# Kernel optimization log

Hardware: AMD Instinct MI355X
Metric: run time of the kernel (lower is better)

## Reference

```python
import jax, jax.numpy as jnp
import numpy as np

N_NODES = 100000


def _gcn_conv(x, row, col, W, b, n):
    # PyG GCNConv: h = W x; out_i = sum_{j->i} norm_ij * h_j + b, with self-loops
    # and symmetric normalization norm_ij = deg_i^-1/2 * deg_j^-1/2.
    h = x @ W  # [N, out]
    loop = jnp.arange(n, dtype=row.dtype)
    r = jnp.concatenate([row, loop])
    c = jnp.concatenate([col, loop])
    deg = jax.ops.segment_sum(jnp.ones_like(c, dtype=h.dtype), c, num_segments=n)
    dinv = jnp.where(deg > 0, jax.lax.rsqrt(deg), 0.0)
    norm = dinv[r] * dinv[c]  # [E+N]
    msg = h[r] * norm[:, None]  # gather + per-edge scale
    out = jax.ops.segment_sum(msg, c, num_segments=n)  # scatter-add to dst
    return out + b


def setup_inputs() -> dict:
    key = jax.random.key(0)
    ks = jax.random.split(key, 8)
    N, E = N_NODES, 1600000
    d_in, comm_dim, hid, out = 120, 8, 128, 64
    x = jax.random.normal(ks[0], (N, d_in), dtype=jnp.float32)
    edge_index = jax.random.randint(ks[1], (2, E), 0, N, dtype=jnp.int64)
    comm_ids = jax.random.randint(ks[2], (N,), 0, 64, dtype=jnp.int64)
    comm_emb = jax.random.normal(ks[3], (64, comm_dim), dtype=jnp.float32)
    s1 = 1.0 / np.sqrt(d_in + comm_dim)
    s2 = 1.0 / np.sqrt(hid)
    W1 = jax.random.normal(ks[4], (d_in + comm_dim, hid), dtype=jnp.float32) * s1
    b1 = jnp.zeros((hid,), dtype=jnp.float32)
    W2 = jax.random.normal(ks[5], (hid, out), dtype=jnp.float32) * s2
    b2 = jnp.zeros((out,), dtype=jnp.float32)
    return {"x": x, "edge_index": edge_index, "comm_ids": comm_ids,
            "comm_emb": comm_emb, "W1": W1, "b1": b1, "W2": W2, "b2": b2}


def reference(x, edge_index, comm_ids, comm_emb, W1, b1, W2, b2):
    n = x.shape[0]
    row, col = edge_index[0], edge_index[1]
    c = comm_emb[comm_ids]                      # [N, comm_dim] embedding lookup
    h = jnp.concatenate([x, c], axis=-1)        # [N, in+comm_dim]
    h = jax.nn.relu(_gcn_conv(h, row, col, W1, b1, n))
    # dropout p=0.5 is inactive in eval mode (training=False)
    out = _gcn_conv(h, row, col, W2, b2, n)     # [N, out_channels]
    return out
```

## Files before the change

kernel.cpp:

```cpp
#include <hip/hip_runtime.h>

typedef __attribute__((ext_vector_type(8))) short bf16x8;
typedef __attribute__((ext_vector_type(4))) float f32x4;

#define CAPB 5632
#define NBMAX 512

static __device__ __forceinline__ unsigned short f2bf(float f) {
    unsigned u = __float_as_uint(f);
    unsigned r = (u + 0x7fff + ((u >> 16) & 1)) >> 16;
    return (unsigned short)r;
}
static __device__ __forceinline__ float bfu_lo(unsigned v) { return __uint_as_float(v << 16); }
static __device__ __forceinline__ float bfu_hi(unsigned v) { return __uint_as_float(v & 0xffff0000u); }

static __device__ __forceinline__ bf16x8 cvt8(float4 u0, float4 u1) {
    bf16x8 r;
    r[0] = (short)f2bf(u0.x); r[1] = (short)f2bf(u0.y);
    r[2] = (short)f2bf(u0.z); r[3] = (short)f2bf(u0.w);
    r[4] = (short)f2bf(u1.x); r[5] = (short)f2bf(u1.y);
    r[6] = (short)f2bf(u1.z); r[7] = (short)f2bf(u1.w);
    return r;
}

__global__ void k_zero_int(int* __restrict__ p, int n) {
    int i = blockIdx.x * blockDim.x + threadIdx.x;
    if (i < n) p[i] = 0;
}

__global__ __launch_bounds__(256) void k_passA(const int* __restrict__ row,
                                               const int* __restrict__ col,
                                               int* __restrict__ gcnt,
                                               unsigned long long* __restrict__ packed,
                                               int E, int NB) {
    __shared__ int lcnt[NBMAX];
    __shared__ int lbase[NBMAX];
    __shared__ int lcur[NBMAX];
    __shared__ int gbaseS[NBMAX];
    __shared__ unsigned long long stage[4096];
    __shared__ int s[256];

    int tid = threadIdx.x;
    int t0 = blockIdx.x * 4096;
    int total = min(4096, E - t0);

    for (int b = tid; b < NBMAX; b += 256) { lcnt[b] = 0; lcur[b] = 0; }
    __syncthreads();

    int er[16], ec[16];
#pragma unroll
    for (int j = 0; j < 16; ++j) {
        int e = t0 + j * 256 + tid;
        if (e < E) {
            er[j] = row[e];
            ec[j] = col[e];
            atomicAdd(&lcnt[ec[j] >> 8], 1);
        }
    }
    __syncthreads();

    int c0 = lcnt[2 * tid], c1 = lcnt[2 * tid + 1];
    int p = c0 + c1;
    s[tid] = p;
    __syncthreads();
    for (int off = 1; off < 256; off <<= 1) {
        int t = (tid >= off) ? s[tid - off] : 0;
        __syncthreads();
        s[tid] += t;
        __syncthreads();
    }
    int ebase = s[tid] - p;
    lbase[2 * tid] = ebase;
    lbase[2 * tid + 1] = ebase + c0;
    __syncthreads();

    for (int b = tid; b < NB; b += 256) {
        int lc = lcnt[b];
        if (lc > 0) gbaseS[b] = atomicAdd(&gcnt[b], lc);
    }
    __syncthreads();

#pragma unroll
    for (int j = 0; j < 16; ++j) {
        int e = t0 + j * 256 + tid;
        if (e < E) {
            int b = ec[j] >> 8;
            int pos = lbase[b] + atomicAdd(&lcur[b], 1);
            stage[pos] = ((unsigned long long)(unsigned)er[j] << 32) | (unsigned)ec[j];
        }
    }
    __syncthreads();

    for (int j = tid; j < total; j += 256) {
        unsigned long long v = stage[j];
        int b = ((int)(unsigned)v) >> 8;
        packed[(size_t)b * CAPB + gbaseS[b] + (j - lbase[b])] = v;
    }
}

__global__ void k_bscan(const int* __restrict__ gcnt, int* __restrict__ gbase,
                        int* __restrict__ indptr, int n, int E, int NB) {
    __shared__ int s[512];
    int tid = threadIdx.x;
    int v = (tid < NB) ? gcnt[tid] : 0;
    s[tid] = v;
    __syncthreads();
    for (int off = 1; off < 512; off <<= 1) {
        int t = (tid >= off) ? s[tid - off] : 0;
        __syncthreads();
        s[tid] += t;
        __syncthreads();
    }
    if (tid < NB) gbase[tid] = s[tid] - v;
    if (tid == 0) indptr[n] = E;
}

__global__ __launch_bounds__(256) void k_passB(const unsigned long long* __restrict__ packed,
                                               const int* __restrict__ gcnt,
                                               const int* __restrict__ gbase,
                                               int* __restrict__ indptr,
                                               float* __restrict__ dinv,
                                               int* __restrict__ srcidx, int n) {
    __shared__ int ncnt[256];
    __shared__ int nbase[256];
    __shared__ int srow[CAPB];

    int b = blockIdx.x;
    int tid = threadIdx.x;
    int nodeBase = b << 8;
    int cntE = min(gcnt[b], CAPB);
    int base = gbase[b];
    size_t pb = (size_t)b * CAPB;

    ncnt[tid] = 0;
    __syncthreads();

    for (int j = tid; j < cntE; j += 256) {
        int c = (int)(unsigned)packed[pb + j];
        atomicAdd(&ncnt[c & 255], 1);
    }
    __syncthreads();

    int v = ncnt[tid];
    nbase[tid] = v;
    __syncthreads();
    for (int off = 1; off < 256; off <<= 1) {
        int t = (tid >= off) ? nbase[tid - off] : 0;
        __syncthreads();
        nbase[tid] += t;
        __syncthreads();
    }
    int excl = nbase[tid] - v;
    __syncthreads();
    nbase[tid] = excl;

    int node = nodeBase + tid;
    if (node < n) {
        indptr[node] = base + excl;
        dinv[node] = rsqrtf((float)(v + 1));
    }
    ncnt[tid] = 0;
    __syncthreads();

    for (int j = tid; j < cntE; j += 256) {
        unsigned long long e = packed[pb + j];
        int c = ((int)(unsigned)e) & 255;
        int r = (int)(e >> 32);
        int p = nbase[c] + atomicAdd(&ncnt[c], 1);
        srow[p] = r;
    }
    __syncthreads();

    for (int j = tid; j < cntE; j += 256) srcidx[base + j] = srow[j];
}

__global__ void k_wprep(const float* __restrict__ W, unsigned short* __restrict__ Wt,
                        int nout) {
    int idx = blockIdx.x * blockDim.x + threadIdx.x;
    if (idx >= nout * 128) return;
    int colc = idx >> 7, k = idx & 127;
    Wt[colc * 128 + k] = f2bf(W[k * nout + colc]);
}

__global__ __launch_bounds__(256) void k_gemm1(const float* __restrict__ x,
                                               const int* __restrict__ cid,
                                               const float* __restrict__ cemb,
                                               const unsigned short* __restrict__ Wt,
                                               const float* __restrict__ dinv,
                                               unsigned short* __restrict__ D, int n) {
    int tid = threadIdx.x;
    int wid = tid >> 6, lane = tid & 63;
    int rbase = blockIdx.x * 64 + wid * 16;
    int lr = lane & 15, kq = lane >> 4;

    int arow = rbase + lr;
    if (arow > n - 1) arow = n - 1;
    const float* xp = x + (size_t)arow * 120 + kq * 8;

    bf16x8 a0 = cvt8(*(const float4*)(xp),      *(const float4*)(xp + 4));
    bf16x8 a1 = cvt8(*(const float4*)(xp + 32), *(const float4*)(xp + 36));
    bf16x8 a2 = cvt8(*(const float4*)(xp + 64), *(const float4*)(xp + 68));
    bf16x8 a3;
    if (kq < 3) {
        a3 = cvt8(*(const float4*)(xp + 96), *(const float4*)(xp + 100));
    } else {
        const float* cp = cemb + (size_t)cid[arow] * 8;
        a3 = cvt8(*(const float4*)(cp), *(const float4*)(cp + 4));
    }

    f32x4 acc[8];
#pragma unroll
    for (int cf = 0; cf < 8; ++cf) acc[cf] = (f32x4){0.f, 0.f, 0.f, 0.f};

#pragma unroll
    for (int cf = 0; cf < 8; ++cf) {
        const unsigned short* bp = Wt + (size_t)(cf * 16 + lr) * 128 + kq * 8;
        bf16x8 b0 = *(const bf16x8*)(bp);
        bf16x8 b1 = *(const bf16x8*)(bp + 32);
        bf16x8 b2 = *(const bf16x8*)(bp + 64);
        bf16x8 b3 = *(const bf16x8*)(bp + 96);
        acc[cf] = __builtin_amdgcn_mfma_f32_16x16x32_bf16(a0, b0, acc[cf], 0, 0, 0);
        acc[cf] = __builtin_amdgcn_mfma_f32_16x16x32_bf16(a1, b1, acc[cf], 0, 0, 0);
        acc[cf] = __builtin_amdgcn_mfma_f32_16x16x32_bf16(a2, b2, acc[cf], 0, 0, 0);
        acc[cf] = __builtin_amdgcn_mfma_f32_16x16x32_bf16(a3, b3, acc[cf], 0, 0, 0);
    }

    float dv[4];
#pragma unroll
    for (int r = 0; r < 4; ++r) {
        int grow = rbase + kq * 4 + r;
        dv[r] = (grow < n) ? dinv[grow] : 0.f;
    }
#pragma unroll
    for (int cf = 0; cf < 8; ++cf) {
#pragma unroll
        for (int r = 0; r < 4; ++r) {
            int grow = rbase + kq * 4 + r;
            if (grow < n) D[(size_t)grow * 128 + cf * 16 + lr] = f2bf(acc[cf][r] * dv[r]);
        }
    }
}

template <int NOUT>
__global__ __launch_bounds__(256) void k_gemm_bf16(const unsigned short* __restrict__ A,
                                                   const unsigned short* __restrict__ Wt,
                                                   const float* __restrict__ dinv,
                                                   unsigned short* __restrict__ D, int n) {
    constexpr int NCF = NOUT / 16;
    int tid = threadIdx.x;
    int wid = tid >> 6, lane = tid & 63;
    int rbase = blockIdx.x * 64 + wid * 16;
    int lr = lane & 15, kq = lane >> 4;

    int arow = rbase + lr;
    if (arow > n - 1) arow = n - 1;
    const unsigned short* ap = A + (size_t)arow * 128 + kq * 8;
    bf16x8 a0 = *(const bf16x8*)(ap);
    bf16x8 a1 = *(const bf16x8*)(ap + 32);
    bf16x8 a2 = *(const bf16x8*)(ap + 64);
    bf16x8 a3 = *(const bf16x8*)(ap + 96);

    f32x4 acc[NCF];
#pragma unroll
    for (int cf = 0; cf < NCF; ++cf) acc[cf] = (f32x4){0.f, 0.f, 0.f, 0.f};

#pragma unroll
    for (int cf = 0; cf < NCF; ++cf) {
        const unsigned short* bp = Wt + (size_t)(cf * 16 + lr) * 128 + kq * 8;
        bf16x8 b0 = *(const bf16x8*)(bp);
        bf16x8 b1 = *(const bf16x8*)(bp + 32);
        bf16x8 b2 = *(const bf16x8*)(bp + 64);
        bf16x8 b3 = *(const bf16x8*)(bp + 96);
        acc[cf] = __builtin_amdgcn_mfma_f32_16x16x32_bf16(a0, b0, acc[cf], 0, 0, 0);
        acc[cf] = __builtin_amdgcn_mfma_f32_16x16x32_bf16(a1, b1, acc[cf], 0, 0, 0);
        acc[cf] = __builtin_amdgcn_mfma_f32_16x16x32_bf16(a2, b2, acc[cf], 0, 0, 0);
        acc[cf] = __builtin_amdgcn_mfma_f32_16x16x32_bf16(a3, b3, acc[cf], 0, 0, 0);
    }

    float dv[4];
#pragma unroll
    for (int r = 0; r < 4; ++r) {
        int grow = rbase + kq * 4 + r;
        dv[r] = (grow < n) ? dinv[grow] : 0.f;
    }
#pragma unroll
    for (int cf = 0; cf < NCF; ++cf) {
#pragma unroll
        for (int r = 0; r < 4; ++r) {
            int grow = rbase + kq * 4 + r;
            if (grow < n) D[(size_t)grow * NOUT + cf * 16 + lr] = f2bf(acc[cf][r] * dv[r]);
        }
    }
}


__global__ __launch_bounds__(64) void k_agg1(const unsigned* __restrict__ Hs,
                                             const int* __restrict__ indptr,
                                             const int* __restrict__ srcidx,
                                             const float* __restrict__ dinv,
                                             const float* __restrict__ bias,
                                             unsigned* __restrict__ Out, int n) {
    int i = blockIdx.x;
    int lane = threadIdx.x;
    unsigned sv = Hs[(size_t)i * 64 + lane];
    float ax = bfu_lo(sv), ay = bfu_hi(sv);
    int e0 = indptr[i], e1 = indptr[i + 1];
#pragma unroll 4
    for (int e = e0; e < e1; ++e) {
        unsigned v = Hs[(size_t)srcidx[e] * 64 + lane];
        ax += bfu_lo(v);
        ay += bfu_hi(v);
    }
    float di = dinv[i];
    float2 b = *(const float2*)&bias[lane * 2];
    float ox = fmaxf(di * ax + b.x, 0.f);
    float oy = fmaxf(di * ay + b.y, 0.f);
    Out[(size_t)i * 64 + lane] = (unsigned)f2bf(ox) | ((unsigned)f2bf(oy) << 16);
}

__global__ __launch_bounds__(64) void k_agg2(const unsigned* __restrict__ Hs,
                                             const int* __restrict__ indptr,
                                             const int* __restrict__ srcidx,
                                             const float* __restrict__ dinv,
                                             const float* __restrict__ bias,
                                             float2* __restrict__ Out, int n) {
    int i = blockIdx.x;
    int lane = threadIdx.x;
    int v = lane & 31, h = lane >> 5;
    float ax = 0.f, ay = 0.f;
    if (h == 0) {
        unsigned sv = Hs[(size_t)i * 32 + v];
        ax = bfu_lo(sv); ay = bfu_hi(sv);
    }
    int e0 = indptr[i], e1 = indptr[i + 1];
#pragma unroll 4
    for (int e = e0 + h; e < e1; e += 2) {
        unsigned w = Hs[(size_t)srcidx[e] * 32 + v];
        ax += bfu_lo(w);
        ay += bfu_hi(w);
    }
    ax += __shfl_xor(ax, 32);
    ay += __shfl_xor(ay, 32);
    if (h == 0) {
        float di = dinv[i];
        float2 b = *(const float2*)&bias[v * 2];
        Out[(size_t)i * 32 + v] = make_float2(di * ax + b.x, di * ay + b.y);
    }
}


extern "C" void kernel_launch(void* const* d_in, const int* in_sizes, int n_in,
                              void* d_out, int out_size, void* d_ws, size_t ws_size,
                              hipStream_t stream) {
    const float* x    = (const float*)d_in[0];
    const int*   eidx = (const int*)d_in[1];
    const int*   cid  = (const int*)d_in[2];
    const float* cemb = (const float*)d_in[3];
    const float* W1   = (const float*)d_in[4];
    const float* b1   = (const float*)d_in[5];
    const float* W2   = (const float*)d_in[6];
    const float* b2   = (const float*)d_in[7];
    float* out = (float*)d_out;

    int n = in_sizes[2];
    int E = in_sizes[1] / 2;
    const int* row = eidx;
    const int* col = eidx + E;
    int NB = (n + 255) / 256;

    char* ws = (char*)d_ws;
    auto alloc = [&](size_t bytes) {
        char* p = ws;
        ws += (bytes + 255) & ~(size_t)255;
        return p;
    };
    float*              dinv   = (float*)alloc((size_t)n * 4);
    int*                gcnt   = (int*)alloc((size_t)NB * 4);
    int*                gbase  = (int*)alloc((size_t)NB * 4);
    int*                indptr = (int*)alloc((size_t)(n + 1) * 4);
    int*                srcidx = (int*)alloc((size_t)E * 4);
    unsigned long long* packed = (unsigned long long*)alloc((size_t)NB * CAPB * 8);
    unsigned short*     Wt1    = (unsigned short*)alloc(128 * 128 * 2);
    unsigned short*     Wt2    = (unsigned short*)alloc(64 * 128 * 2);
    unsigned short*     D1     = (unsigned short*)alloc((size_t)n * 128 * 2);
    unsigned short*     H1     = (unsigned short*)alloc((size_t)n * 128 * 2);
    unsigned short*     D2     = (unsigned short*)alloc((size_t)n * 64 * 2);

    k_zero_int<<<(NB + 255) / 256, 256, 0, stream>>>(gcnt, NB);
    k_passA<<<(E + 4095) / 4096, 256, 0, stream>>>(row, col, gcnt, packed, E, NB);
    k_bscan<<<1, 512, 0, stream>>>(gcnt, gbase, indptr, n, E, NB);
    k_passB<<<NB, 256, 0, stream>>>(packed, gcnt, gbase, indptr, dinv, srcidx, n);

    k_wprep<<<(128 * 128 + 255) / 256, 256, 0, stream>>>(W1, Wt1, 128);
    k_wprep<<<(64 * 128 + 255) / 256, 256, 0, stream>>>(W2, Wt2, 64);

    int gb = (n + 63) / 64;
    k_gemm1<<<gb, 256, 0, stream>>>(x, cid, cemb, Wt1, dinv, D1, n);
    k_agg1<<<n, 64, 0, stream>>>((const unsigned*)D1, indptr, srcidx, dinv, b1,
                                 (unsigned*)H1, n);
    k_gemm_bf16<64><<<gb, 256, 0, stream>>>(H1, Wt2, dinv, D2, n);
    k_agg2<<<n, 64, 0, stream>>>((const unsigned*)D2, indptr, srcidx, dinv, b2,
                                 (float2*)out, n);
}
```

Before: 225.3 us.

## Quantize layer-1 features to int8 with per-row scales and pack edges in 32 bits

The first GEMM now writes its dinv-scaled output as int8 with a per-row absmax scale instead of bf16. This halves the bytes that the layer-1 aggregation gathers per neighbor. The aggregation dequantizes on the fly, writes H1 in a permuted column order, and the W2 weights are permuted to match. Edge packing during the CSR build shrinks from 64-bit to 32-bit words (row<<8 | low col bits), and the two weight-prep launches are merged into one. The cost is lower precision in the layer-1 messages, which may hurt accuracy, plus an extra scale load per edge.

```diff
diff --git a/kernel.cpp b/kernel.cpp
--- a/kernel.cpp
+++ b/kernel.cpp
@@ -13,6 +13,9 @@
 }
 static __device__ __forceinline__ float bfu_lo(unsigned v) { return __uint_as_float(v << 16); }
 static __device__ __forceinline__ float bfu_hi(unsigned v) { return __uint_as_float(v & 0xffff0000u); }
+static __device__ __forceinline__ unsigned packbf(float a, float b) {
+    return (unsigned)f2bf(a) | ((unsigned)f2bf(b) << 16);
+}
 
 static __device__ __forceinline__ bf16x8 cvt8(float4 u0, float4 u1) {
     bf16x8 r;
@@ -31,13 +34,14 @@
 __global__ __launch_bounds__(256) void k_passA(const int* __restrict__ row,
                                                const int* __restrict__ col,
                                                int* __restrict__ gcnt,
-                                               unsigned long long* __restrict__ packed,
+                                               unsigned* __restrict__ packed,
                                                int E, int NB) {
     __shared__ int lcnt[NBMAX];
     __shared__ int lbase[NBMAX];
     __shared__ int lcur[NBMAX];
     __shared__ int gbaseS[NBMAX];
-    __shared__ unsigned long long stage[4096];
+    __shared__ unsigned stage[4096];
+    __shared__ unsigned short stageb[4096];
     __shared__ int s[256];
 
     int tid = threadIdx.x;
@@ -86,15 +90,15 @@
         if (e < E) {
             int b = ec[j] >> 8;
             int pos = lbase[b] + atomicAdd(&lcur[b], 1);
-            stage[pos] = ((unsigned long long)(unsigned)er[j] << 32) | (unsigned)ec[j];
+            stage[pos] = ((unsigned)er[j] << 8) | ((unsigned)ec[j] & 255u);
+            stageb[pos] = (unsigned short)b;
         }
     }
     __syncthreads();
 
     for (int j = tid; j < total; j += 256) {
-        unsigned long long v = stage[j];
-        int b = ((int)(unsigned)v) >> 8;
-        packed[(size_t)b * CAPB + gbaseS[b] + (j - lbase[b])] = v;
+        int b = stageb[j];
+        packed[(size_t)b * CAPB + gbaseS[b] + (j - lbase[b])] = stage[j];
     }
 }
 
@@ -115,7 +119,7 @@
     if (tid == 0) indptr[n] = E;
 }
 
-__global__ __launch_bounds__(256) void k_passB(const unsigned long long* __restrict__ packed,
+__global__ __launch_bounds__(256) void k_passB(const unsigned* __restrict__ packed,
                                                const int* __restrict__ gcnt,
                                                const int* __restrict__ gbase,
                                                int* __restrict__ indptr,
@@ -136,8 +140,8 @@
     __syncthreads();
 
     for (int j = tid; j < cntE; j += 256) {
-        int c = (int)(unsigned)packed[pb + j];
-        atomicAdd(&ncnt[c & 255], 1);
+        unsigned e = packed[pb + j];
+        atomicAdd(&ncnt[e & 255u], 1);
     }
     __syncthreads();
 
@@ -163,9 +167,9 @@
     __syncthreads();
 
     for (int j = tid; j < cntE; j += 256) {
-        unsigned long long e = packed[pb + j];
-        int c = ((int)(unsigned)e) & 255;
-        int r = (int)(e >> 32);
+        unsigned e = packed[pb + j];
+        int c = (int)(e & 255u);
+        int r = (int)(e >> 8);
         int p = nbase[c] + atomicAdd(&ncnt[c], 1);
         srow[p] = r;
     }
@@ -174,12 +178,18 @@
     for (int j = tid; j < cntE; j += 256) srcidx[base + j] = srow[j];
 }
 
-__global__ void k_wprep(const float* __restrict__ W, unsigned short* __restrict__ Wt,
-                        int nout) {
+__global__ void k_wprep(const float* __restrict__ W1, const float* __restrict__ W2,
+                        unsigned short* __restrict__ Wt1, unsigned short* __restrict__ Wt2p) {
     int idx = blockIdx.x * blockDim.x + threadIdx.x;
-    if (idx >= nout * 128) return;
-    int colc = idx >> 7, k = idx & 127;
-    Wt[colc * 128 + k] = f2bf(W[k * nout + colc]);
+    if (idx < 128 * 128) {
+        int colc = idx >> 7, k = idx & 127;
+        Wt1[colc * 128 + k] = f2bf(W1[k * 128 + colc]);
+    } else if (idx < 128 * 128 + 64 * 128) {
+        int j = idx - 128 * 128;
+        int colc = j >> 7, p = j & 127;
+        int korig = (p & 7) * 16 + (p >> 3);
+        Wt2p[colc * 128 + p] = f2bf(W2[korig * 64 + colc]);
+    }
 }
 
 __global__ __launch_bounds__(256) void k_gemm1(const float* __restrict__ x,
@@ -187,7 +197,8 @@
                                                const float* __restrict__ cemb,
                                                const unsigned short* __restrict__ Wt,
                                                const float* __restrict__ dinv,
-                                               unsigned short* __restrict__ D, int n) {
+                                               unsigned char* __restrict__ D1q,
+                                               float* __restrict__ scales, int n) {
     int tid = threadIdx.x;
     int wid = tid >> 6, lane = tid & 63;
     int rbase = blockIdx.x * 64 + wid * 16;
@@ -225,18 +236,32 @@
         acc[cf] = __builtin_amdgcn_mfma_f32_16x16x32_bf16(a3, b3, acc[cf], 0, 0, 0);
     }
 
-    float dv[4];
 #pragma unroll
     for (int r = 0; r < 4; ++r) {
         int grow = rbase + kq * 4 + r;
-        dv[r] = (grow < n) ? dinv[grow] : 0.f;
-    }
-#pragma unroll
-    for (int cf = 0; cf < 8; ++cf) {
-#pragma unroll
-        for (int r = 0; r < 4; ++r) {
-            int grow = rbase + kq * 4 + r;
-            if (grow < n) D[(size_t)grow * 128 + cf * 16 + lr] = f2bf(acc[cf][r] * dv[r]);
+        float dv = (grow < n) ? dinv[grow] : 0.f;
+        float m = 0.f;
+#pragma unroll
+        for (int cf = 0; cf < 8; ++cf) m = fmaxf(m, fabsf(acc[cf][r] * dv));
+        m = fmaxf(m, __shfl_xor(m, 1));
+        m = fmaxf(m, __shfl_xor(m, 2));
+        m = fmaxf(m, __shfl_xor(m, 4));
+        m = fmaxf(m, __shfl_xor(m, 8));
+        float sinv = (m > 1e-20f) ? 127.f / m : 0.f;
+        if (grow < n) {
+            if (lr == 0) scales[grow] = m * (1.f / 127.f);
+            unsigned lo = 0, hi = 0;
+#pragma unroll
+            for (int cf = 0; cf < 4; ++cf) {
+                int q8 = (int)rintf(acc[cf][r] * dv * sinv);
+                lo |= ((unsigned)(q8 & 255)) << (8 * cf);
+            }
+#pragma unroll
+            for (int cf = 4; cf < 8; ++cf) {
+                int q8 = (int)rintf(acc[cf][r] * dv * sinv);
+                hi |= ((unsigned)(q8 & 255)) << (8 * (cf - 4));
+            }
+            *(uint2*)&D1q[(size_t)grow * 128 + lr * 8] = make_uint2(lo, hi);
         }
     }
 }
@@ -293,8 +318,8 @@
     }
 }
 
-
-__global__ __launch_bounds__(64) void k_agg1(const unsigned* __restrict__ Hs,
+__global__ __launch_bounds__(64) void k_agg1(const unsigned char* __restrict__ Hq,
+                                             const float* __restrict__ scales,
                                              const int* __restrict__ indptr,
                                              const int* __restrict__ srcidx,
                                              const float* __restrict__ dinv,
@@ -302,20 +327,27 @@
                                              unsigned* __restrict__ Out, int n) {
     int i = blockIdx.x;
     int lane = threadIdx.x;
-    unsigned sv = Hs[(size_t)i * 64 + lane];
-    float ax = bfu_lo(sv), ay = bfu_hi(sv);
+    int c0 = ((2 * lane) & 7) * 16 + (lane >> 2);
+    float bx = bias[c0], by = bias[c0 + 16];
+    float di = dinv[i];
+
+    unsigned short sq = *(const unsigned short*)(Hq + (size_t)i * 128 + 2 * lane);
+    float ss = scales[i];
+    float ax = ss * (float)(signed char)(sq & 255);
+    float ay = ss * (float)(signed char)(sq >> 8);
+
     int e0 = indptr[i], e1 = indptr[i + 1];
 #pragma unroll 4
     for (int e = e0; e < e1; ++e) {
-        unsigned v = Hs[(size_t)srcidx[e] * 64 + lane];
-        ax += bfu_lo(v);
-        ay += bfu_hi(v);
-    }
-    float di = dinv[i];
-    float2 b = *(const float2*)&bias[lane * 2];
-    float ox = fmaxf(di * ax + b.x, 0.f);
-    float oy = fmaxf(di * ay + b.y, 0.f);
-    Out[(size_t)i * 64 + lane] = (unsigned)f2bf(ox) | ((unsigned)f2bf(oy) << 16);
+        int s = srcidx[e];
+        unsigned short q = *(const unsigned short*)(Hq + (size_t)s * 128 + 2 * lane);
+        float sc = scales[s];
+        ax += sc * (float)(signed char)(q & 255);
+        ay += sc * (float)(signed char)(q >> 8);
+    }
+    float ox = fmaxf(di * ax + bx, 0.f);
+    float oy = fmaxf(di * ay + by, 0.f);
+    Out[(size_t)i * 64 + lane] = packbf(ox, oy);
 }
 
 __global__ __launch_bounds__(64) void k_agg2(const unsigned* __restrict__ Hs,
@@ -327,10 +359,13 @@
     int i = blockIdx.x;
     int lane = threadIdx.x;
     int v = lane & 31, h = lane >> 5;
+    float di = dinv[i];
+    float2 b = *(const float2*)&bias[v * 2];
     float ax = 0.f, ay = 0.f;
     if (h == 0) {
         unsigned sv = Hs[(size_t)i * 32 + v];
-        ax = bfu_lo(sv); ay = bfu_hi(sv);
+        ax = bfu_lo(sv);
+        ay = bfu_hi(sv);
     }
     int e0 = indptr[i], e1 = indptr[i + 1];
 #pragma unroll 4
@@ -342,8 +377,6 @@
     ax += __shfl_xor(ax, 32);
     ay += __shfl_xor(ay, 32);
     if (h == 0) {
-        float di = dinv[i];
-        float2 b = *(const float2*)&bias[v * 2];
         Out[(size_t)i * 32 + v] = make_float2(di * ax + b.x, di * ay + b.y);
     }
 }
@@ -374,31 +407,31 @@
         ws += (bytes + 255) & ~(size_t)255;
         return p;
     };
-    float*              dinv   = (float*)alloc((size_t)n * 4);
-    int*                gcnt   = (int*)alloc((size_t)NB * 4);
-    int*                gbase  = (int*)alloc((size_t)NB * 4);
-    int*                indptr = (int*)alloc((size_t)(n + 1) * 4);
-    int*                srcidx = (int*)alloc((size_t)E * 4);
-    unsigned long long* packed = (unsigned long long*)alloc((size_t)NB * CAPB * 8);
-    unsigned short*     Wt1    = (unsigned short*)alloc(128 * 128 * 2);
-    unsigned short*     Wt2    = (unsigned short*)alloc(64 * 128 * 2);
-    unsigned short*     D1     = (unsigned short*)alloc((size_t)n * 128 * 2);
-    unsigned short*     H1     = (unsigned short*)alloc((size_t)n * 128 * 2);
-    unsigned short*     D2     = (unsigned short*)alloc((size_t)n * 64 * 2);
+    float*          dinv   = (float*)alloc((size_t)n * 4);
+    int*            gcnt   = (int*)alloc((size_t)NB * 4);
+    int*            gbase  = (int*)alloc((size_t)NB * 4);
+    int*            indptr = (int*)alloc((size_t)(n + 1) * 4);
+    int*            srcidx = (int*)alloc((size_t)E * 4);
+    unsigned*       packed = (unsigned*)alloc((size_t)NB * CAPB * 4);
+    unsigned short* Wt1    = (unsigned short*)alloc(128 * 128 * 2);
+    unsigned short* Wt2p   = (unsigned short*)alloc(64 * 128 * 2);
+    unsigned char*  D1q    = (unsigned char*)alloc((size_t)n * 128);
+    float*          scales = (float*)alloc((size_t)n * 4);
+    unsigned short* H1p    = (unsigned short*)alloc((size_t)n * 128 * 2);
+    unsigned short* D2     = (unsigned short*)alloc((size_t)n * 64 * 2);
 
     k_zero_int<<<(NB + 255) / 256, 256, 0, stream>>>(gcnt, NB);
     k_passA<<<(E + 4095) / 4096, 256, 0, stream>>>(row, col, gcnt, packed, E, NB);
     k_bscan<<<1, 512, 0, stream>>>(gcnt, gbase, indptr, n, E, NB);
     k_passB<<<NB, 256, 0, stream>>>(packed, gcnt, gbase, indptr, dinv, srcidx, n);
 
-    k_wprep<<<(128 * 128 + 255) / 256, 256, 0, stream>>>(W1, Wt1, 128);
-    k_wprep<<<(64 * 128 + 255) / 256, 256, 0, stream>>>(W2, Wt2, 64);
+    k_wprep<<<(128 * 128 + 64 * 128 + 255) / 256, 256, 0, stream>>>(W1, W2, Wt1, Wt2p);
 
     int gb = (n + 63) / 64;
-    k_gemm1<<<gb, 256, 0, stream>>>(x, cid, cemb, Wt1, dinv, D1, n);
-    k_agg1<<<n, 64, 0, stream>>>((const unsigned*)D1, indptr, srcidx, dinv, b1,
-                                 (unsigned*)H1, n);
-    k_gemm_bf16<64><<<gb, 256, 0, stream>>>(H1, Wt2, dinv, D2, n);
+    k_gemm1<<<gb, 256, 0, stream>>>(x, cid, cemb, Wt1, dinv, D1q, scales, n);
+    k_agg1<<<n, 64, 0, stream>>>(D1q, scales, indptr, srcidx, dinv, b1,
+                                 (unsigned*)H1p, n);
+    k_gemm_bf16<64><<<gb, 256, 0, stream>>>(H1p, Wt2p, dinv, D2, n);
     k_agg2<<<n, 64, 0, stream>>>((const unsigned*)D2, indptr, srcidx, dinv, b2,
                                  (float2*)out, n);
 }
```

After: 213.2 us. -5.3%, faster.
